# Optimization experiments

Hardware: AMD Instinct MI355X
Metric: run time of the kernel (lower is better)

## Reference

```python
import jax, jax.numpy as jnp
import numpy as np

N_STIMULI = 10000
N_DIM = 128
N_GROUP = 4
BATCH = 65536
N_REF = 8      # n_max_reference
N_SEL = 2      # n_max_select
RHO = 2.0      # Minkowski exponent (psiz ExponentialKernel default)
TAU = 1.0      # similarity exponent
BETA = 10.0    # similarity decay rate
GAMMA = 0.0    # similarity baseline


def setup_inputs() -> dict:
    key = jax.random.key(0)
    k1, k2, k3, k4 = jax.random.split(key, 4)
    stimulus_set = jax.random.randint(k1, (BATCH, N_REF + 1), 0, N_STIMULI, dtype=jnp.int32)
    membership = jax.random.randint(k2, (BATCH, 2), 0, N_GROUP, dtype=jnp.int32)
    is_present = jnp.ones((BATCH, N_REF + 1), dtype=bool)
    is_select = jnp.ones((BATCH, N_SEL), dtype=bool)
    z = jax.random.normal(k3, (N_STIMULI, N_DIM), dtype=jnp.float32) * 0.1
    w = jax.random.uniform(k4, (N_GROUP, N_DIM), dtype=jnp.float32, minval=0.5, maxval=1.5)
    return {"stimulus_set": stimulus_set, "membership": membership,
            "is_present": is_present, "is_select": is_select, "z": z, "w": w}


def _forward(stimulus_set, membership, is_present, is_select, z, w):
    group_id = membership[:, 0]                      # (B,)
    att = w[group_id]                                # (B, D) attention weights
    zset = z[stimulus_set]                           # (B, R+1, D)
    z_q = zset[:, :1, :]                             # (B, 1, D) query
    z_r = zset[:, 1:, :]                             # (B, R, D) references
    # weighted Minkowski distance over embedding dim
    diff = jnp.abs(z_q - z_r)                        # (B, R, D)
    d = jnp.sum(att[:, None, :] * diff ** RHO, axis=-1) ** (1.0 / RHO)  # (B, R)
    sim_qr = jnp.exp(-BETA * d ** TAU) + GAMMA       # (B, R)
    sim_qr = sim_qr * is_present[:, 1:].astype(sim_qr.dtype)
    # ranked sequence probability. The TF loop maintains
    # denom(i) = sum_{j>=i} sim_qr[:, j], i.e. a reverse cumulative sum.
    n_sel = is_select.shape[1]
    denom = jnp.cumsum(sim_qr[:, ::-1], axis=1)[:, ::-1]  # (B, R)
    denom_s = denom[:, :n_sel]                       # (B, S)
    num = sim_qr[:, :n_sel]                          # (B, S)
    safe = jnp.where(denom_s == 0.0, 1.0, denom_s)
    prob = jnp.where(denom_s == 0.0, 0.0, num / safe)  # divide_no_nan
    sel = is_select.astype(prob.dtype)
    prob = prob * sel + (1.0 - sel)
    return jnp.prod(prob, axis=1)                    # (B,)


def reference(stimulus_set, membership, is_present, is_select, z, w):
    return _forward(stimulus_set, membership, is_present, is_select, z, w)
```

## Files before the change

kernel.cpp:

```cpp
#include <hip/hip_runtime.h>

typedef _Float16 h2 __attribute__((ext_vector_type(2)));

#define NDIM  128
#define NSTIM 10000
#define NG    4
#define ZH_BYTES (NSTIM * NDIM * 2)

union U4H8 { uint4 u; h2 h[4]; };

static __device__ __forceinline__ float fdot2(h2 a, h2 b, float c) {
#if __has_builtin(__builtin_amdgcn_fdot2)
    return __builtin_amdgcn_fdot2(a, b, c, false);
#else
    return c + ((float)a[0] * (float)b[0] + (float)a[1] * (float)b[1]);
#endif
}

__global__ __launch_bounds__(256) void zconv_k(
    const float* __restrict__ z, const float* __restrict__ w,
    _Float16* __restrict__ zh, _Float16* __restrict__ wh)
{
    const int tid = blockIdx.x * blockDim.x + threadIdx.x;
    if (tid < NG * NDIM / 4) {
        const float4 v = reinterpret_cast<const float4*>(w)[tid];
        h2 a; a.x = (_Float16)v.x; a.y = (_Float16)v.y;
        h2 b; b.x = (_Float16)v.z; b.y = (_Float16)v.w;
        uint2 p; p.x = *(unsigned int*)&a; p.y = *(unsigned int*)&b;
        reinterpret_cast<uint2*>(wh)[tid] = p;
    }
    if (tid < NSTIM * NDIM / 4) {
        const float4 v = reinterpret_cast<const float4*>(z)[tid];
        h2 a; a.x = (_Float16)v.x; a.y = (_Float16)v.y;
        h2 b; b.x = (_Float16)v.z; b.y = (_Float16)v.w;
        uint2 p; p.x = *(unsigned int*)&a; p.y = *(unsigned int*)&b;
        reinterpret_cast<uint2*>(zh)[tid] = p;
    }
}

__global__ __launch_bounds__(256) void rank8_k(
    const int* __restrict__ stim, const int* __restrict__ membership,
    const _Float16* __restrict__ zh, const _Float16* __restrict__ wh,
    float* __restrict__ out)
{
    const int lane = threadIdx.x & 63;
    const int li = lane & 7;
    const int row = (blockIdx.x * 4 + (threadIdx.x >> 6)) * 8 + (lane >> 3);

    const int* ss = stim + row * 9;
    int sid[9];
#pragma unroll
    for (int i = 0; i < 9; ++i) sid[i] = ss[i];
    const int grp = membership[row * 2];

#define ZROW(s) (zh + (size_t)(s) * NDIM + li * 8)

    U4H8 qb0, qb1, zb[5][2];
    qb0.u = *(const uint4*)ZROW(sid[0]);
    qb1.u = *(const uint4*)(ZROW(sid[0]) + 64);
#pragma unroll
    for (int r = 0; r < 5; ++r) {
        zb[r][0].u = *(const uint4*)ZROW(sid[r + 1]);
        zb[r][1].u = *(const uint4*)(ZROW(sid[r + 1]) + 64);
    }

    const _Float16* wrow = wh + grp * NDIM + li * 8;
    U4H8 wb0, wb1;
    wb0.u = *(const uint4*)wrow;
    wb1.u = *(const uint4*)(wrow + 64);

    float dot[8];
#pragma unroll
    for (int r = 0; r < 8; ++r) {
        const U4H8 z0 = zb[r % 5][0], z1 = zb[r % 5][1];
        float a = 0.0f;
#pragma unroll
        for (int j = 0; j < 4; ++j) {
            h2 t = qb0.h[j] - z0.h[j];
            h2 wt = wb0.h[j] * t;
            a = fdot2(wt, t, a);
        }
#pragma unroll
        for (int j = 0; j < 4; ++j) {
            h2 t = qb1.h[j] - z1.h[j];
            h2 wt = wb1.h[j] * t;
            a = fdot2(wt, t, a);
        }
        dot[r] = a;
        if (r + 5 < 8) {
            zb[r][0].u = *(const uint4*)ZROW(sid[r + 6]);
            zb[r][1].u = *(const uint4*)(ZROW(sid[r + 6]) + 64);
        }
    }
#undef ZROW

    float t4[4];
    {
        const bool hi = (li & 4) != 0;
#pragma unroll
        for (int j = 0; j < 4; ++j) {
            const float keep = hi ? dot[j + 4] : dot[j];
            const float send = hi ? dot[j] : dot[j + 4];
            t4[j] = keep + __shfl_xor(send, 4, 64);
        }
    }
    float t2[2];
    {
        const bool hi = (li & 2) != 0;
#pragma unroll
        for (int j = 0; j < 2; ++j) {
            const float keep = hi ? t4[j + 2] : t4[j];
            const float send = hi ? t4[j] : t4[j + 2];
            t2[j] = keep + __shfl_xor(send, 2, 64);
        }
    }
    float d2;
    {
        const bool hi = (li & 1) != 0;
        const float keep = hi ? t2[1] : t2[0];
        const float send = hi ? t2[0] : t2[1];
        d2 = keep + __shfl_xor(send, 1, 64);
    }

    d2 = fmaxf(d2, 0.0f);
    const float d = __builtin_amdgcn_sqrtf(d2);
    const float sim = __expf(-10.0f * d);

    float den1 = (li == 0) ? 0.0f : sim;
    den1 += __shfl_xor(den1, 1, 64);
    den1 += __shfl_xor(den1, 2, 64);
    den1 += __shfl_xor(den1, 4, 64);

    const int base = lane & 56;
    const float s0 = __shfl(sim, base + 0, 64);
    const float s1 = __shfl(sim, base + 1, 64);
    const float p0 = __fdividef(s0, den1 + s0);
    const float p1 = __fdividef(s1, den1);
    if (li == 0) out[row] = p0 * p1;
}

extern "C" void kernel_launch(void* const* d_in, const int* in_sizes, int n_in,
                              void* d_out, int out_size, void* d_ws, size_t ws_size,
                              hipStream_t stream) {
    const int* stim = (const int*)d_in[0];
    const int* membership = (const int*)d_in[1];
    const float* z = (const float*)d_in[4];
    const float* w = (const float*)d_in[5];
    float* out = (float*)d_out;

    char* ws = (char*)d_ws;
    _Float16* zh = (_Float16*)ws;
    _Float16* wh = (_Float16*)(ws + ZH_BYTES);

    zconv_k<<<(NSTIM * NDIM / 4 + 255) / 256, 256, 0, stream>>>(z, w, zh, wh);
    rank8_k<<<2048, 256, 0, stream>>>(stim, membership, zh, wh, out);
}
```

Before: 19.51 us.

## Expand weighted distance into precomputed norms minus cross term

The prep kernel now also computes a per-stimulus, per-group weighted squared norm table S[g][s] = sum w*z^2 alongside the fp16 conversion. The main kernel rewrites d2 as Sq + Sr - 2*sum(w*q*r), precomputing w*q once so each reference needs one packed dot per pair instead of subtract, multiply and dot. This cuts the inner-loop ALU work at the cost of an extra gathered table read per lane. It also adds cancellation risk, since fp16 products are subtracted from fp32 norms.

```diff
diff --git a/kernel.cpp b/kernel.cpp
--- a/kernel.cpp
+++ b/kernel.cpp
@@ -6,6 +6,7 @@
 #define NSTIM 10000
 #define NG    4
 #define ZH_BYTES (NSTIM * NDIM * 2)
+#define S_BYTES  (NG * NSTIM * 4)
 
 union U4H8 { uint4 u; h2 h[4]; };
 
@@ -17,31 +18,73 @@
 #endif
 }
 
-__global__ __launch_bounds__(256) void zconv_k(
+__global__ __launch_bounds__(256) void prepx_k(
     const float* __restrict__ z, const float* __restrict__ w,
-    _Float16* __restrict__ zh, _Float16* __restrict__ wh)
+    _Float16* __restrict__ zh, float* __restrict__ Stab,
+    _Float16* __restrict__ wh)
 {
     const int tid = blockIdx.x * blockDim.x + threadIdx.x;
-    if (tid < NG * NDIM / 4) {
-        const float4 v = reinterpret_cast<const float4*>(w)[tid];
-        h2 a; a.x = (_Float16)v.x; a.y = (_Float16)v.y;
-        h2 b; b.x = (_Float16)v.z; b.y = (_Float16)v.w;
-        uint2 p; p.x = *(unsigned int*)&a; p.y = *(unsigned int*)&b;
-        reinterpret_cast<uint2*>(wh)[tid] = p;
-    }
-    if (tid < NSTIM * NDIM / 4) {
-        const float4 v = reinterpret_cast<const float4*>(z)[tid];
-        h2 a; a.x = (_Float16)v.x; a.y = (_Float16)v.y;
-        h2 b; b.x = (_Float16)v.z; b.y = (_Float16)v.w;
-        uint2 p; p.x = *(unsigned int*)&a; p.y = *(unsigned int*)&b;
-        reinterpret_cast<uint2*>(zh)[tid] = p;
-    }
-}
-
-__global__ __launch_bounds__(256) void rank8_k(
+    if (tid < NG * NDIM) wh[tid] = (_Float16)w[tid];
+
+    const int lane = threadIdx.x & 63;
+    const int li = lane & 7;
+    const int s = (blockIdx.x * 4 + (threadIdx.x >> 6)) * 8 + (lane >> 3);
+    if (s >= NSTIM) return;
+
+    const float* zrow = z + (size_t)s * NDIM + li * 8;
+    float zf[16];
+    *(float4*)(zf)      = *(const float4*)(zrow);
+    *(float4*)(zf + 4)  = *(const float4*)(zrow + 4);
+    *(float4*)(zf + 8)  = *(const float4*)(zrow + 64);
+    *(float4*)(zf + 12) = *(const float4*)(zrow + 68);
+
+    h2 zp[8];
+#pragma unroll
+    for (int j = 0; j < 8; ++j) {
+        h2 v; v.x = (_Float16)zf[2 * j]; v.y = (_Float16)zf[2 * j + 1];
+        zp[j] = v;
+    }
+
+    U4H8 o0, o1;
+#pragma unroll
+    for (int j = 0; j < 4; ++j) { o0.h[j] = zp[j]; o1.h[j] = zp[4 + j]; }
+    _Float16* zd = zh + (size_t)s * NDIM + li * 8;
+    *(uint4*)zd        = o0.u;
+    *(uint4*)(zd + 64) = o1.u;
+
+    float acc[NG];
+#pragma unroll
+    for (int g = 0; g < NG; ++g) {
+        const float* wrow = w + g * NDIM + li * 8;
+        float wf[16];
+        *(float4*)(wf)      = *(const float4*)(wrow);
+        *(float4*)(wf + 4)  = *(const float4*)(wrow + 4);
+        *(float4*)(wf + 8)  = *(const float4*)(wrow + 64);
+        *(float4*)(wf + 12) = *(const float4*)(wrow + 68);
+        float a = 0.0f;
+#pragma unroll
+        for (int j = 0; j < 8; ++j) {
+            h2 wp; wp.x = (_Float16)wf[2 * j]; wp.y = (_Float16)wf[2 * j + 1];
+            h2 wz = wp * zp[j];
+            a = fdot2(wz, zp[j], a);
+        }
+        acc[g] = a;
+    }
+#pragma unroll
+    for (int m = 4; m >= 1; m >>= 1) {
+#pragma unroll
+        for (int g = 0; g < NG; ++g) acc[g] += __shfl_xor(acc[g], m, 64);
+    }
+    if (li == 0) {
+#pragma unroll
+        for (int g = 0; g < NG; ++g) Stab[g * NSTIM + s] = acc[g];
+    }
+}
+
+__global__ __launch_bounds__(256) void rankx_k(
     const int* __restrict__ stim, const int* __restrict__ membership,
-    const _Float16* __restrict__ zh, const _Float16* __restrict__ wh,
-    float* __restrict__ out)
+    const _Float16* __restrict__ zh, const float* __restrict__ Stab,
+    const _Float16* __restrict__ wh, float* __restrict__ out)
 {
     const int lane = threadIdx.x & 63;
     const int li = lane & 7;
@@ -53,6 +96,9 @@
     for (int i = 0; i < 9; ++i) sid[i] = ss[i];
     const int grp = membership[row * 2];
 
+    const float Sq = Stab[grp * NSTIM + sid[0]];
+    const float Sr = Stab[grp * NSTIM + sid[li + 1]];
+
 #define ZROW(s) (zh + (size_t)(s) * NDIM + li * 8)
 
     U4H8 qb0, qb1, zb[5][2];
@@ -69,23 +115,22 @@
     wb0.u = *(const uint4*)wrow;
     wb1.u = *(const uint4*)(wrow + 64);
 
+    h2 wq[8];
+#pragma unroll
+    for (int j = 0; j < 4; ++j) {
+        wq[j]     = wb0.h[j] * qb0.h[j];
+        wq[4 + j] = wb1.h[j] * qb1.h[j];
+    }
+
     float dot[8];
 #pragma unroll
     for (int r = 0; r < 8; ++r) {
         const U4H8 z0 = zb[r % 5][0], z1 = zb[r % 5][1];
         float a = 0.0f;
 #pragma unroll
-        for (int j = 0; j < 4; ++j) {
-            h2 t = qb0.h[j] - z0.h[j];
-            h2 wt = wb0.h[j] * t;
-            a = fdot2(wt, t, a);
-        }
-#pragma unroll
-        for (int j = 0; j < 4; ++j) {
-            h2 t = qb1.h[j] - z1.h[j];
-            h2 wt = wb1.h[j] * t;
-            a = fdot2(wt, t, a);
-        }
+        for (int j = 0; j < 4; ++j) a = fdot2(wq[j], z0.h[j], a);
+#pragma unroll
+        for (int j = 0; j < 4; ++j) a = fdot2(wq[4 + j], z1.h[j], a);
         dot[r] = a;
         if (r + 5 < 8) {
             zb[r][0].u = *(const uint4*)ZROW(sid[r + 6]);
@@ -114,14 +159,15 @@
             t2[j] = keep + __shfl_xor(send, 2, 64);
         }
     }
-    float d2;
+    float dfull;
     {
         const bool hi = (li & 1) != 0;
         const float keep = hi ? t2[1] : t2[0];
         const float send = hi ? t2[0] : t2[1];
-        d2 = keep + __shfl_xor(send, 1, 64);
-    }
-
+        dfull = keep + __shfl_xor(send, 1, 64);
+    }
+
+    float d2 = (Sq + Sr) - 2.0f * dfull;
     d2 = fmaxf(d2, 0.0f);
     const float d = __builtin_amdgcn_sqrtf(d2);
     const float sim = __expf(-10.0f * d);
@@ -150,8 +196,9 @@
 
     char* ws = (char*)d_ws;
     _Float16* zh = (_Float16*)ws;
-    _Float16* wh = (_Float16*)(ws + ZH_BYTES);
-
-    zconv_k<<<(NSTIM * NDIM / 4 + 255) / 256, 256, 0, stream>>>(z, w, zh, wh);
-    rank8_k<<<2048, 256, 0, stream>>>(stim, membership, zh, wh, out);
-}
+    float* Stab = (float*)(ws + ZH_BYTES);
+    _Float16* wh = (_Float16*)(ws + ZH_BYTES + S_BYTES);
+
+    prepx_k<<<313, 256, 0, stream>>>(z, w, zh, Stab, wh);
+    rankx_k<<<2048, 256, 0, stream>>>(stim, membership, zh, Stab, wh, out);
+}
```

New measurement: 21.55 us. +10.5%, slower.
